# Optimization experiments

Hardware: AMD Instinct MI355X
Metric: run time of the kernel (lower is better)

## Reference

```python
import jax, jax.numpy as jnp
import numpy as np
import math

B, S, D = 4, 1024, 1024
H, DK = 16, 64
NUM_BUCKETS, MAX_DIST = 32, 128


def _relative_position_bucket(relative_position, num_buckets=NUM_BUCKETS, max_distance=MAX_DIST):
    # bidirectional bucketing (T5 encoder style)
    num_buckets = num_buckets // 2
    buckets = (relative_position > 0).astype(jnp.int32) * num_buckets
    rp = jnp.abs(relative_position)
    max_exact = num_buckets // 2
    is_small = rp < max_exact
    # clamp to >=1 to avoid log(0); masked out by is_small anyway
    rp_large = max_exact + (
        jnp.log(jnp.maximum(rp, 1).astype(jnp.float32) / max_exact)
        / math.log(max_distance / max_exact)
        * (num_buckets - max_exact)
    ).astype(jnp.int32)
    rp_large = jnp.minimum(rp_large, num_buckets - 1)
    return buckets + jnp.where(is_small, rp, rp_large)


def compute_bias(rel_bias_table, q_len, k_len):
    ctx = jnp.arange(q_len)[:, None]
    mem = jnp.arange(k_len)[None, :]
    buckets = _relative_position_bucket(mem - ctx)  # [q,k]
    values = rel_bias_table[buckets]  # [q,k,H]
    return jnp.transpose(values, (2, 0, 1))  # [H,q,k]


def setup_inputs() -> dict:
    key = jax.random.key(0)
    ks = jax.random.split(key, 6)
    return {
        "hidden_states": jax.random.normal(ks[0], (B, S, D), dtype=jnp.float32),
        "Wq": jax.random.normal(ks[1], (D, H * DK), dtype=jnp.float32) * 0.02,
        "Wk": jax.random.normal(ks[2], (D, H * DK), dtype=jnp.float32) * 0.02,
        "Wv": jax.random.normal(ks[3], (D, H * DK), dtype=jnp.float32) * 0.02,
        "Wo": jax.random.normal(ks[4], (H * DK, D), dtype=jnp.float32) * 0.02,
        "rel_bias_table": jax.random.normal(ks[5], (NUM_BUCKETS, H), dtype=jnp.float32),
    }


def reference(hidden_states, Wq, Wk, Wv, Wo, rel_bias_table):
    b, s, _ = hidden_states.shape
    # projections (no bias), split heads -> [b,h,s,dk]
    def heads(x):
        return jnp.transpose(x.reshape(b, s, H, DK), (0, 2, 1, 3))
    q = heads(hidden_states @ Wq)
    k = heads(hidden_states @ Wk)
    v = heads(hidden_states @ Wv)
    # NOTE: T5 attention is UNSCALED (no 1/sqrt(dk))
    scores = jnp.einsum("bhqd,bhkd->bhqk", q, k)
    bias = compute_bias(rel_bias_table, s, s)[None]  # [1,H,s,s]
    scores = scores + bias
    attn = jax.nn.softmax(scores.astype(jnp.float32), axis=-1).astype(scores.dtype)
    out = jnp.einsum("bhqk,bhkd->bhqd", attn, v)
    out = jnp.transpose(out, (0, 2, 1, 3)).reshape(b, s, H * DK)
    return out @ Wo
```

## Files before the change

kernel.cpp:

```cpp
#include <hip/hip_runtime.h>
#include <hip/hip_bf16.h>

typedef __attribute__((ext_vector_type(8))) short short8;
typedef __attribute__((ext_vector_type(4))) float f32x4;
typedef unsigned short u16;

#define AS1 __attribute__((address_space(1)))
#define AS3 __attribute__((address_space(3)))

#define LOG2E 1.44269504088896f
#define FOLD_M 46.166241308446828f
#define EXP2(x) __builtin_amdgcn_exp2f(x)

__device__ __forceinline__ u16 f2bf(float f) {
    unsigned u = __builtin_bit_cast(unsigned, f);
    u += 0x7FFFu + ((u >> 16) & 1u);
    return (u16)(u >> 16);
}

__device__ __forceinline__ unsigned pk2(float a, float b) {
    unsigned ua = __builtin_bit_cast(unsigned, a) + 0x8000u;
    unsigned ub = __builtin_bit_cast(unsigned, b) + 0x8000u;
    return __builtin_amdgcn_perm(ub, ua, 0x07060302);
}

__global__ __launch_bounds__(256) void k_f32_to_bf16(const float* __restrict__ in,
                                                     u16* __restrict__ out, int n4) {
    int i = blockIdx.x * 256 + threadIdx.x;
    if (i < n4) {
        float4 v = ((const float4*)in)[i];
        ushort4 o;
        o.x = f2bf(v.x); o.y = f2bf(v.y); o.z = f2bf(v.z); o.w = f2bf(v.w);
        ((ushort4*)out)[i] = o;
    }
}

__global__ __launch_bounds__(256) void k_prep(const float* __restrict__ Wq, const float* __restrict__ Wk,
                                              const float* __restrict__ Wv, const float* __restrict__ Wo,
                                              const float* __restrict__ tbl,
                                              u16* __restrict__ wt, u16* __restrict__ wot,
                                              float* __restrict__ bias2) {
    int z = blockIdx.z;
    if (z == 4) {
        int idx = (blockIdx.y * 32 + blockIdx.x) * 256 + threadIdx.x;
        if (idx < 16 * 2048) {
            int r = idx & 2047, h = idx >> 11;
            int rel = r - 1023;
            int bucket = rel > 0 ? 16 : 0;
            int rp = rel < 0 ? -rel : rel;
            if (rp < 8) bucket += rp;
            else {
                int lb = 8 + (int)(log2f((float)rp * 0.125f) * 2.0f);
                bucket += (lb < 15 ? lb : 15);
            }
            bias2[idx] = tbl[bucket * 16 + h] * LOG2E - FOLD_M;
        }
        return;
    }
    const float* in = z == 0 ? Wq : z == 1 ? Wk : z == 2 ? Wv : Wo;
    u16* out = (z == 3) ? wot : wt + (size_t)z * 1024 * 1024;
    __shared__ float tile[32][33];
    int tx = threadIdx.x & 31, ty = threadIdx.x >> 5;
    int bx = blockIdx.x << 5, by = blockIdx.y << 5;
    #pragma unroll
    for (int j = 0; j < 32; j += 8)
        tile[ty + j][tx] = in[(size_t)(by + ty + j) * 1024 + bx + tx];
    __syncthreads();
    #pragma unroll
    for (int j = 0; j < 32; j += 8)
        out[(size_t)(bx + ty + j) * 1024 + by + tx] = f2bf(tile[tx][ty + j]);
}

template<int MODE>
__global__ __launch_bounds__(256) void k_gemm(const u16* __restrict__ A, const u16* __restrict__ Bt,
                                              u16* __restrict__ oq, u16* __restrict__ ok,
                                              u16* __restrict__ ov, float* __restrict__ outf,
                                              int N, int K) {
    __shared__ u16 As[128 * 32];
    __shared__ u16 Bs[128 * 32];
    int t = threadIdx.x, lane = t & 63, wave = t >> 6;
    int m0 = blockIdx.y << 7, n0 = blockIdx.x << 7;
    int wm = (wave >> 1) << 6, wn = (wave & 1) << 6;
    f32x4 acc[4][4];
    #pragma unroll
    for (int i = 0; i < 4; i++)
        #pragma unroll
        for (int j = 0; j < 4; j++) acc[i][j] = (f32x4){0.f, 0.f, 0.f, 0.f};

    const u16* gA = A + (size_t)(m0 + wave * 16 + (lane >> 2)) * K + ((lane & 3) << 3);
    const u16* gB = Bt + (size_t)(n0 + wave * 16 + (lane >> 2)) * K + ((lane & 3) << 3);
    int ldsOff = wave * 16 * 32;

    for (int k0 = 0; k0 < K; k0 += 32) {
        __syncthreads();
        __builtin_amdgcn_global_load_lds((const AS1 void*)(gA + k0),           (AS3 void*)&As[ldsOff],           16, 0, 0);
        __builtin_amdgcn_global_load_lds((const AS1 void*)(gA + 64 * K + k0),  (AS3 void*)&As[ldsOff + 64 * 32], 16, 0, 0);
        __builtin_amdgcn_global_load_lds((const AS1 void*)(gB + k0),           (AS3 void*)&Bs[ldsOff],           16, 0, 0);
        __builtin_amdgcn_global_load_lds((const AS1 void*)(gB + 64 * K + k0),  (AS3 void*)&Bs[ldsOff + 64 * 32], 16, 0, 0);
        __syncthreads();
        short8 af[4], bfr[4];
        #pragma unroll
        for (int fm = 0; fm < 4; fm++)
            af[fm] = *(const short8*)&As[(wm + (fm << 4) + (lane & 15)) * 32 + ((lane >> 4) << 3)];
        #pragma unroll
        for (int fn = 0; fn < 4; fn++)
            bfr[fn] = *(const short8*)&Bs[(wn + (fn << 4) + (lane & 15)) * 32 + ((lane >> 4) << 3)];
        #pragma unroll
        for (int fm = 0; fm < 4; fm++)
            #pragma unroll
            for (int fn = 0; fn < 4; fn++)
                acc[fm][fn] = __builtin_amdgcn_mfma_f32_16x16x32_bf16(af[fm], bfr[fn], acc[fm][fn], 0, 0, 0);
    }
    #pragma unroll
    for (int fm = 0; fm < 4; fm++)
        #pragma unroll
        for (int fn = 0; fn < 4; fn++) {
            int mb = m0 + wm + (fm << 4) + ((lane >> 4) << 2);
            int n = n0 + wn + (fn << 4) + (lane & 15);
            if (MODE == 0) {
                int j = n >> 10, col = n & 1023;
                int h = col >> 6, dk = col & 63;
                int b = mb >> 10, s = mb & 1023;
                if (j == 2) {
                    ushort4 pk;
                    pk.x = f2bf(acc[fm][fn][0]); pk.y = f2bf(acc[fm][fn][1]);
                    pk.z = f2bf(acc[fm][fn][2]); pk.w = f2bf(acc[fm][fn][3]);
                    *(ushort4*)(ov + ((size_t)(((b << 4) + h) * 64 + dk)) * 1024 + s) = pk;
                } else {
                    u16* dst = (j == 0) ? oq : ok;
                    #pragma unroll
                    for (int r = 0; r < 4; r++)
                        dst[((size_t)(((b << 4) + h) * 1024 + s + r)) * 64 + dk] = f2bf(acc[fm][fn][r]);
                }
            } else {
                #pragma unroll
                for (int r = 0; r < 4; r++)
                    outf[(size_t)(mb + r) * N + n] = acc[fm][fn][r];
            }
        }
}

__global__ __launch_bounds__(256, 2) void k_attn(const u16* __restrict__ Qg, const u16* __restrict__ Kg,
                                                 const u16* __restrict__ Vtg, const float* __restrict__ bias2,
                                                 u16* __restrict__ attn_out) {
    __shared__ __align__(16) u16 Ks[2][64 * 64];
    __shared__ __align__(16) u16 Vts[2][64 * 64];
    __shared__ __align__(16) u16 Ps[128 * 64];
    __shared__ __align__(16) float blds4[4][1160];

    int t = threadIdx.x, lane = t & 63, w = t >> 6;
    int bid = blockIdx.x;
    int sid = (bid & 7) * 64 + (bid >> 3);
    int qb = sid & 7, h = (sid >> 3) & 15, b = sid >> 7;
    int q0 = qb << 7;
    const u16* Qh = Qg + ((size_t)(((b << 4) + h) * 1024 + q0)) * 64;
    const u16* Kh = Kg + (size_t)(((b << 4) + h)) * 1024 * 64;
    const u16* Vth = Vtg + (size_t)(((b << 4) + h)) * 64 * 1024;
    const float* bh = bias2 + (h << 11);

    int g = lane >> 4, ln = lane & 15;
    int swz = (ln & 7) << 4;

    short8 qf[2][2];
    #pragma unroll
    for (int fm = 0; fm < 2; fm++)
        #pragma unroll
        for (int kh = 0; kh < 2; kh++)
            qf[fm][kh] = *(const short8*)(Qh + (size_t)(w * 32 + fm * 16 + ln) * 64 + kh * 32 + g * 8);

    int w0 = 896 - q0;
    for (int i = t; i < 1152; i += 256) {
        float v = bh[w0 + i];
        #pragma unroll
        for (int a2 = 0; a2 < 4; a2++) { int x = i - a2; if (x >= 0) blds4[a2][x] = v; }
    }
    float b_hi = bh[1023 + 256];
    float b_lo = bh[1023 - 256];
    int aRep = (3 - ln) & 3;
    const float* repB = &blds4[aRep][0];

    #define STAGE(kb_, buf_)                                                                     \
        {                                                                                        \
            _Pragma("unroll")                                                                    \
            for (int r2 = 0; r2 < 2; r2++) {                                                     \
                int L = t * 16 + r2 * 4096;                                                      \
                int row = L >> 7, gI = (L >> 4) & 7, gp = gI ^ (row & 7);                        \
                __builtin_amdgcn_global_load_lds(                                                \
                    (const AS1 void*)(Kh + (size_t)((kb_) * 64 + row) * 64 + gp * 8),            \
                    (AS3 void*)&Ks[buf_][L >> 1], 16, 0, 0);                                     \
                __builtin_amdgcn_global_load_lds(                                                \
                    (const AS1 void*)(Vth + (size_t)row * 1024 + (kb_) * 64 + gp * 8),           \
                    (AS3 void*)&Vts[buf_][L >> 1], 16, 0, 0);                                    \
            }                                                                                    \
        }

    STAGE(0, 0);
    __syncthreads();

    float psum[2] = {0.f, 0.f};
    f32x4 o[2][4];
    #pragma unroll
    for (int fm = 0; fm < 2; fm++)
        #pragma unroll
        for (int dn = 0; dn < 4; dn++) o[fm][dn] = (f32x4){0.f, 0.f, 0.f, 0.f};

    #pragma unroll 2
    for (int kb = 0; kb < 16; kb++) {
        const int cur = kb & 1;
        if (kb < 15) STAGE(kb + 1, cur ^ 1);

        f32x4 s[2][4];
        __builtin_amdgcn_s_setprio(1);
        #pragma unroll
        for (int fn = 0; fn < 4; fn++) {
            int row = (fn << 4) + ln;
            short8 kf0 = *(const short8*)((const char*)Ks[cur] + row * 128 + (((g << 4) + 0)  ^ ((row & 7) << 4)));
            short8 kf1 = *(const short8*)((const char*)Ks[cur] + row * 128 + (((g << 4) + 64) ^ ((row & 7) << 4)));
            #pragma unroll
            for (int fm = 0; fm < 2; fm++) {
                f32x4 a = (f32x4){0.f, 0.f, 0.f, 0.f};
                a = __builtin_amdgcn_mfma_f32_16x16x32_bf16(kf0, qf[fm][0], a, 0, 0, 0);
                a = __builtin_amdgcn_mfma_f32_16x16x32_bf16(kf1, qf[fm][1], a, 0, 0, 0);
                s[fm][fn] = a;
            }
        }
        __builtin_amdgcn_s_setprio(0);

        int d0 = 64 * kb - q0 - 32 * w;
        int ibase = 64 * kb - 32 * w + 127 + 4 * g - ln;
        bool fast = (d0 >= 122) || (d0 <= -154);
        float bu = d0 > 0 ? b_hi : b_lo;
        #pragma unroll
        for (int fm = 0; fm < 2; fm++) {
            int prow = 32 * w + 16 * fm + ln;
            #pragma unroll
            for (int fn = 0; fn < 4; fn++) {
                f32x4 sv = s[fm][fn];
                float b0, b1, b2v, b3;
                if (fast) { b0 = b1 = b2v = b3 = bu; }
                else {
                    float4 bb = *(const float4*)(repB + (ibase + 16 * fn - 16 * fm - aRep));
                    b0 = bb.x; b1 = bb.y; b2v = bb.z; b3 = bb.w;
                }
                float p0 = EXP2(fmaf(sv[0], LOG2E, b0));
                float p1 = EXP2(fmaf(sv[1], LOG2E, b1));
                float p2 = EXP2(fmaf(sv[2], LOG2E, b2v));
                float p3 = EXP2(fmaf(sv[3], LOG2E, b3));
                psum[fm] += (p0 + p1) + (p2 + p3);
                uint2 pv;
                pv.x = pk2(p0, p1);
                pv.y = pk2(p2, p3);
                *(uint2*)((char*)Ps + prow * 128 + (((fn << 5) + (g << 3)) ^ swz)) = pv;
            }
        }

        short8 pa[2][2];
        #pragma unroll
        for (int fm = 0; fm < 2; fm++) {
            int prow = 32 * w + 16 * fm + ln;
            #pragma unroll
            for (int kh = 0; kh < 2; kh++)
                pa[fm][kh] = *(const short8*)((const char*)Ps + prow * 128 + (((kh << 6) + (g << 4)) ^ swz));
        }
        __builtin_amdgcn_s_setprio(1);
        #pragma unroll
        for (int dn = 0; dn < 4; dn++) {
            int vrow = (dn << 4) + ln;
            short8 vb0 = *(const short8*)((const char*)Vts[cur] + vrow * 128 + (((g << 4) + 0)  ^ ((vrow & 7) << 4)));
            short8 vb1 = *(const short8*)((const char*)Vts[cur] + vrow * 128 + (((g << 4) + 64) ^ ((vrow & 7) << 4)));
            #pragma unroll
            for (int fm = 0; fm < 2; fm++) {
                f32x4 a = o[fm][dn];
                a = __builtin_amdgcn_mfma_f32_16x16x32_bf16(pa[fm][0], vb0, a, 0, 0, 0);
                a = __builtin_amdgcn_mfma_f32_16x16x32_bf16(pa[fm][1], vb1, a, 0, 0, 0);
                o[fm][dn] = a;
            }
        }
        __builtin_amdgcn_s_setprio(0);

        __syncthreads();
    }

    float linv[2][4];
    #pragma unroll
    for (int fm = 0; fm < 2; fm++) {
        float v = psum[fm];
        v += __shfl_xor(v, 16);
        v += __shfl_xor(v, 32);
        float inv = 1.0f / v;
        #pragma unroll
        for (int r = 0; r < 4; r++)
            linv[fm][r] = __shfl(inv, 4 * g + r);
    }
    #pragma unroll
    for (int fm = 0; fm < 2; fm++)
        #pragma unroll
        for (int dn = 0; dn < 4; dn++)
            #pragma unroll
            for (int r = 0; r < 4; r++) {
                int srow = q0 + 32 * w + 16 * fm + (g << 2) + r;
                int col = (h << 6) + (dn << 4) + ln;
                attn_out[((size_t)((b << 10) + srow) << 10) + col] = f2bf(o[fm][dn][r] * linv[fm][r]);
            }
}

extern "C" void kernel_launch(void* const* d_in, const int* in_sizes, int n_in,
                              void* d_out, int out_size, void* d_ws, size_t ws_size,
                              hipStream_t stream) {
    const float* hidden = (const float*)d_in[0];
    const float* Wq = (const float*)d_in[1];
    const float* Wk = (const float*)d_in[2];
    const float* Wv = (const float*)d_in[3];
    const float* Wo = (const float*)d_in[4];
    const float* tbl = (const float*)d_in[5];

    u16* hidb = (u16*)d_ws;
    u16* wt   = hidb + 4096 * 1024;
    u16* wot  = wt + 3072 * 1024;
    u16* Qb   = wot + 1024 * 1024;
    u16* Kb   = Qb + 4 * 16 * 1024 * 64;
    u16* Vb   = Kb + 4 * 16 * 1024 * 64;
    u16* attn = Vb + 4 * 16 * 1024 * 64;
    float* bias = (float*)(attn + 4096 * 1024);

    k_f32_to_bf16<<<4096, 256, 0, stream>>>(hidden, hidb, 4096 * 1024 / 4);
    k_prep<<<dim3(32, 32, 5), 256, 0, stream>>>(Wq, Wk, Wv, Wo, tbl, wt, wot, bias);
    k_gemm<0><<<dim3(24, 32), 256, 0, stream>>>(hidb, wt, Qb, Kb, Vb, nullptr, 3072, 1024);
    k_attn<<<512, 256, 0, stream>>>(Qb, Kb, Vb, bias, attn);
    k_gemm<1><<<dim3(8, 32), 256, 0, stream>>>(attn, wot, nullptr, nullptr, nullptr,
                                               (float*)d_out, 1024, 1024);
}
```

Baseline: 115.6 us.

## Double-buffer GEMM LDS tiles, swizzle LDS chunks, fuse hidden cast into prep

The GEMM kernel now double-buffers its LDS tiles, prefetching the next K slice while MFMAs run on the current one, which cuts the loop to one barrier per step. It also XOR-swizzles the 16-byte chunks within each LDS row to reduce bank conflicts on fragment reads. The output projection uses a half-height M tile (64 rows) so it launches twice as many blocks for better CU occupancy. The fp32-to-bf16 cast of the hidden states is folded into the prep kernel as extra z-slices, saving one launch. In exchange, LDS use doubles and K is hardcoded to 1024.

```diff
diff --git a/kernel.cpp b/kernel.cpp
--- a/kernel.cpp
+++ b/kernel.cpp
@@ -24,23 +24,22 @@
     return __builtin_amdgcn_perm(ub, ua, 0x07060302);
 }
 
-__global__ __launch_bounds__(256) void k_f32_to_bf16(const float* __restrict__ in,
-                                                     u16* __restrict__ out, int n4) {
-    int i = blockIdx.x * 256 + threadIdx.x;
-    if (i < n4) {
-        float4 v = ((const float4*)in)[i];
-        ushort4 o;
-        o.x = f2bf(v.x); o.y = f2bf(v.y); o.z = f2bf(v.z); o.w = f2bf(v.w);
-        ((ushort4*)out)[i] = o;
-    }
-}
-
-__global__ __launch_bounds__(256) void k_prep(const float* __restrict__ Wq, const float* __restrict__ Wk,
+__global__ __launch_bounds__(256) void k_prep(const float* __restrict__ hidden,
+                                              const float* __restrict__ Wq, const float* __restrict__ Wk,
                                               const float* __restrict__ Wv, const float* __restrict__ Wo,
                                               const float* __restrict__ tbl,
+                                              u16* __restrict__ hidb,
                                               u16* __restrict__ wt, u16* __restrict__ wot,
                                               float* __restrict__ bias2) {
     int z = blockIdx.z;
+    if (z >= 5) {
+        int i = ((z - 5) * 1024 + blockIdx.y * 32 + blockIdx.x) * 256 + threadIdx.x;
+        float4 v = ((const float4*)hidden)[i];
+        ushort4 o;
+        o.x = f2bf(v.x); o.y = f2bf(v.y); o.z = f2bf(v.z); o.w = f2bf(v.w);
+        ((ushort4*)hidb)[i] = o;
+        return;
+    }
     if (z == 4) {
         int idx = (blockIdx.y * 32 + blockIdx.x) * 256 + threadIdx.x;
         if (idx < 16 * 2048) {
@@ -71,52 +70,74 @@
         out[(size_t)(bx + ty + j) * 1024 + by + tx] = f2bf(tile[tx][ty + j]);
 }
 
-template<int MODE>
+template<int MODE, int FM>
 __global__ __launch_bounds__(256) void k_gemm(const u16* __restrict__ A, const u16* __restrict__ Bt,
                                               u16* __restrict__ oq, u16* __restrict__ ok,
                                               u16* __restrict__ ov, float* __restrict__ outf,
-                                              int N, int K) {
-    __shared__ u16 As[128 * 32];
-    __shared__ u16 Bs[128 * 32];
+                                              int N) {
+    const int K = 1024;
+    __shared__ u16 As[2][FM * 1024];
+    __shared__ u16 Bs[2][4096];
     int t = threadIdx.x, lane = t & 63, wave = t >> 6;
-    int m0 = blockIdx.y << 7, n0 = blockIdx.x << 7;
-    int wm = (wave >> 1) << 6, wn = (wave & 1) << 6;
-    f32x4 acc[4][4];
-    #pragma unroll
-    for (int i = 0; i < 4; i++)
+    int m0 = blockIdx.y * (FM * 32), n0 = blockIdx.x << 7;
+    int wm = (wave >> 1) * (FM * 16), wn = (wave & 1) << 6;
+    int g = lane >> 4, ln = lane & 15;
+    f32x4 acc[FM][4];
+    #pragma unroll
+    for (int i = 0; i < FM; i++)
         #pragma unroll
         for (int j = 0; j < 4; j++) acc[i][j] = (f32x4){0.f, 0.f, 0.f, 0.f};
 
-    const u16* gA = A + (size_t)(m0 + wave * 16 + (lane >> 2)) * K + ((lane & 3) << 3);
-    const u16* gB = Bt + (size_t)(n0 + wave * 16 + (lane >> 2)) * K + ((lane & 3) << 3);
-    int ldsOff = wave * 16 * 32;
-
-    for (int k0 = 0; k0 < K; k0 += 32) {
-        __syncthreads();
-        __builtin_amdgcn_global_load_lds((const AS1 void*)(gA + k0),           (AS3 void*)&As[ldsOff],           16, 0, 0);
-        __builtin_amdgcn_global_load_lds((const AS1 void*)(gA + 64 * K + k0),  (AS3 void*)&As[ldsOff + 64 * 32], 16, 0, 0);
-        __builtin_amdgcn_global_load_lds((const AS1 void*)(gB + k0),           (AS3 void*)&Bs[ldsOff],           16, 0, 0);
-        __builtin_amdgcn_global_load_lds((const AS1 void*)(gB + 64 * K + k0),  (AS3 void*)&Bs[ldsOff + 64 * 32], 16, 0, 0);
-        __syncthreads();
-        short8 af[4], bfr[4];
-        #pragma unroll
-        for (int fm = 0; fm < 4; fm++)
-            af[fm] = *(const short8*)&As[(wm + (fm << 4) + (lane & 15)) * 32 + ((lane >> 4) << 3)];
+    int schunk = ((lane & 3) ^ ((lane >> 3) & 3)) << 3;
+    const u16* gA = A + (size_t)(m0 + wave * 16 + (lane >> 2)) * K + schunk;
+    const u16* gB = Bt + (size_t)(n0 + wave * 16 + (lane >> 2)) * K + schunk;
+    int ldsOff = wave * 512;
+
+    #define GSTAGE(k0_, buf_)                                                                          \
+        {                                                                                              \
+            __builtin_amdgcn_global_load_lds((const AS1 void*)(gA + (k0_)),                            \
+                                             (AS3 void*)&As[buf_][ldsOff], 16, 0, 0);                  \
+            if (FM == 4)                                                                               \
+                __builtin_amdgcn_global_load_lds((const AS1 void*)(gA + 64 * K + (k0_)),               \
+                                                 (AS3 void*)&As[buf_][ldsOff + 2048], 16, 0, 0);       \
+            __builtin_amdgcn_global_load_lds((const AS1 void*)(gB + (k0_)),                            \
+                                             (AS3 void*)&Bs[buf_][ldsOff], 16, 0, 0);                  \
+            __builtin_amdgcn_global_load_lds((const AS1 void*)(gB + 64 * K + (k0_)),                   \
+                                             (AS3 void*)&Bs[buf_][ldsOff + 2048], 16, 0, 0);           \
+        }
+
+    GSTAGE(0, 0);
+    __syncthreads();
+
+    int rchunk = (g ^ ((ln >> 1) & 3)) << 3;
+
+    #pragma unroll 2
+    for (int kb = 0; kb < 32; kb++) {
+        const int cur = kb & 1;
+        if (kb < 31) GSTAGE((kb + 1) * 32, cur ^ 1);
+
+        short8 af[FM], bfr[4];
+        #pragma unroll
+        for (int fm = 0; fm < FM; fm++)
+            af[fm] = *(const short8*)&As[cur][(wm + (fm << 4) + ln) * 32 + rchunk];
         #pragma unroll
         for (int fn = 0; fn < 4; fn++)
-            bfr[fn] = *(const short8*)&Bs[(wn + (fn << 4) + (lane & 15)) * 32 + ((lane >> 4) << 3)];
-        #pragma unroll
-        for (int fm = 0; fm < 4; fm++)
+            bfr[fn] = *(const short8*)&Bs[cur][(wn + (fn << 4) + ln) * 32 + rchunk];
+        #pragma unroll
+        for (int fm = 0; fm < FM; fm++)
             #pragma unroll
             for (int fn = 0; fn < 4; fn++)
                 acc[fm][fn] = __builtin_amdgcn_mfma_f32_16x16x32_bf16(af[fm], bfr[fn], acc[fm][fn], 0, 0, 0);
-    }
-    #pragma unroll
-    for (int fm = 0; fm < 4; fm++)
+
+        __syncthreads();
+    }
+
+    #pragma unroll
+    for (int fm = 0; fm < FM; fm++)
         #pragma unroll
         for (int fn = 0; fn < 4; fn++) {
-            int mb = m0 + wm + (fm << 4) + ((lane >> 4) << 2);
-            int n = n0 + wn + (fn << 4) + (lane & 15);
+            int mb = m0 + wm + (fm << 4) + (g << 2);
+            int n = n0 + wn + (fn << 4) + ln;
             if (MODE == 0) {
                 int j = n >> 10, col = n & 1023;
                 int h = col >> 6, dk = col & 63;
@@ -138,6 +159,7 @@
                     outf[(size_t)(mb + r) * N + n] = acc[fm][fn][r];
             }
         }
+    #undef GSTAGE
 }
 
 __global__ __launch_bounds__(256, 2) void k_attn(const u16* __restrict__ Qg, const u16* __restrict__ Kg,
@@ -323,10 +345,9 @@
     u16* attn = Vb + 4 * 16 * 1024 * 64;
     float* bias = (float*)(attn + 4096 * 1024);
 
-    k_f32_to_bf16<<<4096, 256, 0, stream>>>(hidden, hidb, 4096 * 1024 / 4);
-    k_prep<<<dim3(32, 32, 5), 256, 0, stream>>>(Wq, Wk, Wv, Wo, tbl, wt, wot, bias);
-    k_gemm<0><<<dim3(24, 32), 256, 0, stream>>>(hidb, wt, Qb, Kb, Vb, nullptr, 3072, 1024);
+    k_prep<<<dim3(32, 32, 9), 256, 0, stream>>>(hidden, Wq, Wk, Wv, Wo, tbl, hidb, wt, wot, bias);
+    k_gemm<0, 4><<<dim3(24, 32), 256, 0, stream>>>(hidb, wt, Qb, Kb, Vb, nullptr, 3072);
     k_attn<<<512, 256, 0, stream>>>(Qb, Kb, Vb, bias, attn);
-    k_gemm<1><<<dim3(8, 32), 256, 0, stream>>>(attn, wot, nullptr, nullptr, nullptr,
-                                               (float*)d_out, 1024, 1024);
-}
+    k_gemm<1, 2><<<dim3(8, 64), 256, 0, stream>>>(attn, wot, nullptr, nullptr, nullptr,
+                                                  (float*)d_out, 1024);
+}
```

New measurement: 102.9 us. 1.12x faster.
